# Optimization experiments

Measured on AMD Instinct MI355X. Metric: run time of the kernel, lower is better.

Reference implementation:

```python
import jax, jax.numpy as jnp
import numpy as np

B, T, S0 = 8, 4, 4096
D_MODEL, H, D, R, RANK = 2048, 16, 128, 64, 512
C = D - R  # content dim = 64


def _rope(x, positions):
    # x: [B, H, T, R]; rotate-half style RoPE as in the torch module
    half = x.shape[-1] // 2
    inv_freq = 1.0 / (10000.0 ** (jnp.arange(half, dtype=jnp.float32) / half))
    freqs = positions.astype(jnp.float32)[:, None] * inv_freq[None, :]  # [T, half]
    cos = jnp.cos(freqs)[None, None].astype(x.dtype)
    sin = jnp.sin(freqs)[None, None].astype(x.dtype)
    x1, x2 = x[..., :half], x[..., half:]
    return jnp.concatenate([x1 * cos - x2 * sin, x1 * sin + x2 * cos], axis=-1)


def setup_inputs() -> dict:
    key = jax.random.key(0)
    ks = jax.random.split(key, 9)
    s = 0.02
    return {
        "x": jax.random.normal(ks[0], (B, T, D_MODEL), jnp.float32),
        "cache_c_kv": jax.random.normal(ks[1], (B, S0, RANK), jnp.float32),
        "cache_k_rope": jax.random.normal(ks[2], (B, S0, H, R), jnp.float32),
        "w_q": jax.random.normal(ks[3], (D_MODEL, H * C), jnp.float32) * s,
        "w_q_rope": jax.random.normal(ks[4], (D_MODEL, H * R), jnp.float32) * s,
        "w_kv_down": jax.random.normal(ks[5], (D_MODEL, RANK), jnp.float32) * s,
        "w_kv_up": jax.random.normal(ks[6], (RANK, H * D), jnp.float32) * s,
        "w_k_rope": jax.random.normal(ks[7], (D_MODEL, H * R), jnp.float32) * s,
        "w_out": jax.random.normal(ks[8], (H * D, D_MODEL), jnp.float32) * s,
    }


def reference(x, cache_c_kv, cache_k_rope, w_q, w_q_rope, w_kv_down, w_kv_up, w_k_rope, w_out):
    cache_len = cache_c_kv.shape[1]
    positions = jnp.arange(cache_len, cache_len + T)

    # queries
    q_content = (x @ w_q).reshape(B, T, H, C).transpose(0, 2, 1, 3)        # [B,H,T,C]
    q_rope = (x @ w_q_rope).reshape(B, T, H, R).transpose(0, 2, 1, 3)      # [B,H,T,R]
    q_rope = _rope(q_rope, positions)
    q = jnp.concatenate([q_content, q_rope], axis=-1)                       # [B,H,T,D]

    # new compressed kv + rope keys, append to cache
    c_kv_new = x @ w_kv_down                                                # [B,T,RANK]
    k_rope_new = (x @ w_k_rope).reshape(B, T, H, R).transpose(0, 2, 1, 3)
    k_rope_new = _rope(k_rope_new, positions).transpose(0, 2, 1, 3)         # [B,T,H,R]
    c_kv = jnp.concatenate([cache_c_kv, c_kv_new], axis=1)                  # [B,S,RANK]
    k_rope = jnp.concatenate([cache_k_rope, k_rope_new], axis=1)            # [B,S,H,R]

    # decompress full cache every step (the expensive MLA pattern)
    S = c_kv.shape[1]
    kv = (c_kv @ w_kv_up).reshape(B, S, H, D)                               # [B,S,H,D]
    k_content = kv[..., :C].transpose(0, 2, 1, 3)                           # [B,H,S,C]
    v = kv.transpose(0, 2, 1, 3)                                            # [B,H,S,D]
    k = jnp.concatenate([k_content, k_rope.transpose(0, 2, 1, 3)], axis=-1) # [B,H,S,D]

    # kv_cache present => is_prefill False => no causal mask (faithful to source)
    scale = 1.0 / jnp.sqrt(jnp.asarray(D, dtype=q.dtype))
    scores = jnp.einsum('bhtd,bhsd->bhts', q, k) * scale
    attn = jax.nn.softmax(scores, axis=-1)
    out = jnp.einsum('bhts,bhsd->bhtd', attn, v)                            # [B,H,T,D]
    out = out.transpose(0, 2, 1, 3).reshape(B, T, H * D)
    return out @ w_out                                                       # [B,T,D_MODEL]
```

## Files before the change

kernel.cpp:

```cpp
#include <hip/hip_runtime.h>
#include <hip/hip_fp16.h>
#include <cmath>

#define BB 8
#define TT 4
#define HH 16
#define DDIM 128
#define RRDIM 64
#define CCDIM 64
#define RANKC 512
#define DMODEL 2048
#define S0C 4096
#define NQ 64
#define HD 2048
#define NACT 3584
#define NSC 65
#define NG 17
#define SPAD 4160
#define SCALE_ATT 0.08838834764831845f

typedef __attribute__((ext_vector_type(8))) short bf16x8;
typedef __attribute__((ext_vector_type(4))) float f32x4;
typedef unsigned short ushortT;

#define AIDX(row, kk) ((row)*132 + (((row)>>2)<<2) + (kk))

static __device__ __forceinline__ unsigned short f2bf(float x) {
  unsigned u = __float_as_uint(x);
  u += 0x7FFFu + ((u >> 16) & 1u);
  return (unsigned short)(u >> 16);
}
static __device__ __forceinline__ unsigned pk2(float a, float b) {
  return (unsigned)f2bf(a) | ((unsigned)f2bf(b) << 16);
}
static __device__ __forceinline__ bf16x8 cvt8(const float4 a, const float4 b) {
  union { uint4 u; bf16x8 h; } r;
  r.u = make_uint4(pk2(a.x, a.y), pk2(a.z, a.w), pk2(b.x, b.y), pk2(b.z, b.w));
  return r.h;
}

__global__ __launch_bounds__(256) void k_front(const float* __restrict__ A,
                                               const float* __restrict__ w0,
                                               const float* __restrict__ w1,
                                               const float* __restrict__ w2,
                                               const float* __restrict__ w3,
                                               const float* __restrict__ cckv,
                                               float* __restrict__ part,
                                               ushortT* __restrict__ ckvT,
                                               float* __restrict__ ckvn) {
  __shared__ float shf[4352];
  const int tid = threadIdx.x;
  const int bx = blockIdx.x;
  if (bx < 448) {
    const int cb = bx % 28;
    const int k0 = (bx / 28) * 128;
    const float* W; int N, lc0, off;
    if (cb < 8)       { W = w0; N = 1024; lc0 = cb * 128;        off = 0; }
    else if (cb < 16) { W = w1; N = 1024; lc0 = (cb - 8) * 128;  off = 1024; }
    else if (cb < 20) { W = w2; N = 512;  lc0 = (cb - 16) * 128; off = 2048; }
    else              { W = w3; N = 1024; lc0 = (cb - 20) * 128; off = 2560; }
    {
      const int row = tid >> 3;
      const int kseg = (tid & 7) * 16;
      const float4* s4 = reinterpret_cast<const float4*>(A + (size_t)row * DMODEL + k0 + kseg);
      float4 v0 = s4[0], v1 = s4[1], v2 = s4[2], v3 = s4[3];
      *reinterpret_cast<float4*>(&shf[AIDX(row, kseg)])      = v0;
      *reinterpret_cast<float4*>(&shf[AIDX(row, kseg + 4)])  = v1;
      *reinterpret_cast<float4*>(&shf[AIDX(row, kseg + 8)])  = v2;
      *reinterpret_cast<float4*>(&shf[AIDX(row, kseg + 12)]) = v3;
    }
    __syncthreads();
    const int cg = tid & 31;
    const int rg = tid >> 5;
    float acc[4][4];
    #pragma unroll
    for (int r = 0; r < 4; ++r)
      #pragma unroll
      for (int c = 0; c < 4; ++c) acc[r][c] = 0.f;
    #pragma unroll 4
    for (int kk = 0; kk < 128; ++kk) {
      const float4 w4 = *reinterpret_cast<const float4*>(W + (size_t)(k0 + kk) * N + lc0 + cg * 4);
      const float wv[4] = {w4.x, w4.y, w4.z, w4.w};
      #pragma unroll
      for (int r = 0; r < 4; ++r) {
        const float av = shf[AIDX(rg * 4 + r, kk)];
        #pragma unroll
        for (int c = 0; c < 4; ++c) acc[r][c] = fmaf(av, wv[c], acc[r][c]);
      }
    }
    #pragma unroll
    for (int r = 0; r < 4; ++r) {
      float4 o = make_float4(acc[r][0], acc[r][1], acc[r][2], acc[r][3]);
      *reinterpret_cast<float4*>(part + ((size_t)(bx / 28) * 32 + rg * 4 + r) * NACT + off + lc0 + cg * 4) = o;
    }
  } else if (bx < 960) {
    ushortT* tlds = reinterpret_cast<ushortT*>(shf);
    const int idx = bx - 448;
    const int b = idx >> 6, c = idx & 63;
    const float* src = cckv + ((size_t)b * S0C + c * 64) * RANKC;
    ushortT* dstT = ckvT + ((size_t)(b * NSC + c) * RANKC) * 64;
    const int s = tid >> 2, rq = tid & 3;
    const int rloc = tid >> 1, shalf = (tid & 1) * 32;
    for (int slab = 0; slab < 4; ++slab) {
      const int r0 = slab * 128;
      #pragma unroll
      for (int i = 0; i < 8; ++i) {
        const float4 v = *reinterpret_cast<const float4*>(src + (size_t)s * RANKC + r0 + rq * 32 + i * 4);
        *reinterpret_cast<uint2*>(&tlds[s * 136 + rq * 32 + i * 4]) =
            make_uint2(pk2(v.x, v.y), pk2(v.z, v.w));
      }
      __syncthreads();
      unsigned pkv[16];
      #pragma unroll
      for (int k = 0; k < 16; ++k) {
        const unsigned t0 = tlds[(shalf + 2 * k)     * 136 + rloc];
        const unsigned t1 = tlds[(shalf + 2 * k + 1) * 136 + rloc];
        pkv[k] = t0 | (t1 << 16);
      }
      uint4* d = reinterpret_cast<uint4*>(dstT + ((size_t)(r0 + rloc)) * 64 + shalf);
      d[0] = make_uint4(pkv[0], pkv[1], pkv[2], pkv[3]);
      d[1] = make_uint4(pkv[4], pkv[5], pkv[6], pkv[7]);
      d[2] = make_uint4(pkv[8], pkv[9], pkv[10], pkv[11]);
      d[3] = make_uint4(pkv[12], pkv[13], pkv[14], pkv[15]);
      __syncthreads();
    }
  } else {
    const int b = bx - 960;
    const uint4 z = make_uint4(0, 0, 0, 0);
    uint4* p = reinterpret_cast<uint4*>(ckvT + ((size_t)(b * NSC + 64) * RANKC) * 64);
    for (int i = tid; i < 4096; i += 256) p[i] = z;
    uint4* q = reinterpret_cast<uint4*>(ckvn + ((size_t)b * 64 + 4) * RANKC);
    for (int i = tid; i < 7680; i += 256) q[i] = z;
  }
}

__global__ __launch_bounds__(256) void k_mid(const float* __restrict__ part0,
                                             const float* __restrict__ cache_kr,
                                             const float* __restrict__ wup,
                                             ushortT* __restrict__ qlat,
                                             float* __restrict__ ckvn,
                                             ushortT* __restrict__ ckvT,
                                             __half* __restrict__ rs) {
  __shared__ float smid[10880];
  const int tid = threadIdx.x;
  const int bx = blockIdx.x;
  if (bx < 1152) {
    const int bh = bx / 9, sy = bx % 9;
    const int b = bh >> 4, h = bh & 15;
    float* raw_q = smid;
    float* raw_k = smid + 256;
    float* qr_l  = smid + 512;
    float* kr_l  = smid + 768;
    {
      const int t = tid >> 6, j = tid & 63;
      const size_t rowoff = (size_t)(b * TT + t) * NACT;
      float sq = 0.f, sk = 0.f;
      #pragma unroll 4
      for (int ks = 0; ks < 16; ++ks) {
        const float* pp = part0 + (size_t)ks * (32 * NACT) + rowoff;
        sq += pp[1024 + h * 64 + j];
        sk += pp[2560 + h * 64 + j];
      }
      raw_q[t * 64 + j] = sq;
      raw_k[t * 64 + j] = sk;
    }
    __syncthreads();
    {
      const int t = tid >> 6, j = tid & 63;
      const int j2 = j & 31;
      const double inv = pow(10000.0, -(double)j2 / 32.0);
      const double fr = (double)(S0C + t) * inv;
      const float cs = (float)cos(fr), sn = (float)sin(fr);
      const float qa = raw_q[t * 64 + j], qp = raw_q[t * 64 + (j ^ 32)];
      const float ka = raw_k[t * 64 + j], kp = raw_k[t * 64 + (j ^ 32)];
      float qv, kv;
      if (j < 32) { qv = qa * cs - qp * sn; kv = ka * cs - kp * sn; }
      else        { qv = qp * sn + qa * cs; kv = kp * sn + ka * cs; }
      qr_l[t * 64 + j] = qv * SCALE_ATT;
      kr_l[t * 64 + j] = kv;
    }
    __syncthreads();
    const int ql = tid & 3;
    float4 qf[4][4];
    #pragma unroll
    for (int t = 0; t < 4; ++t)
      #pragma unroll
      for (int u = 0; u < 4; ++u)
        qf[t][u] = *reinterpret_cast<const float4*>(&qr_l[t * 64 + ql * 16 + u * 4]);
    const int s0 = sy * 512;
    #pragma unroll 1
    for (int pass = 0; pass < 8; ++pass) {
      const int s = s0 + pass * 64 + (tid >> 2);
      if (s < 4100) {
        float p[4] = {0.f, 0.f, 0.f, 0.f};
        if (s < S0C) {
          const float* krow = cache_kr + (((size_t)b * S0C + s) * HH + h) * RRDIM;
          #pragma unroll
          for (int u = 0; u < 4; ++u) {
            const float4 kv = *reinterpret_cast<const float4*>(krow + ql * 16 + u * 4);
            #pragma unroll
            for (int t = 0; t < 4; ++t)
              p[t] += kv.x * qf[t][u].x + kv.y * qf[t][u].y
                    + kv.z * qf[t][u].z + kv.w * qf[t][u].w;
          }
        } else {
          const float* krow = &kr_l[(s - S0C) * 64];
          #pragma unroll
          for (int u = 0; u < 4; ++u) {
            const float4 kv = *reinterpret_cast<const float4*>(krow + ql * 16 + u * 4);
            #pragma unroll
            for (int t = 0; t < 4; ++t)
              p[t] += kv.x * qf[t][u].x + kv.y * qf[t][u].y
                    + kv.z * qf[t][u].z + kv.w * qf[t][u].w;
          }
        }
        #pragma unroll
        for (int t = 0; t < 4; ++t) {
          p[t] += __shfl_xor(p[t], 1, 4);
          p[t] += __shfl_xor(p[t], 2, 4);
        }
        rs[((size_t)bh * 4 + ql) * SPAD + s] = __float2half(p[ql]);
      }
    }
  } else if (bx < 1216) {
    const int lx = bx - 1152;
    const int h = lx & 15;
    const int r0 = (lx >> 4) * 128;
    float* wt  = smid;
    float* a_s = smid + 8448;
    {
      const int r = tid >> 1;
      const int cseg = (tid & 1) * 32;
      const float* src = wup + (size_t)(r0 + r) * HD + h * DDIM + cseg;
      #pragma unroll
      for (int u = 0; u < 8; ++u) {
        const float4 v = *reinterpret_cast<const float4*>(src + u * 4);
        wt[(cseg + u * 4 + 0) * 132 + r] = v.x;
        wt[(cseg + u * 4 + 1) * 132 + r] = v.y;
        wt[(cseg + u * 4 + 2) * 132 + r] = v.z;
        wt[(cseg + u * 4 + 3) * 132 + r] = v.w;
      }
    }
    {
      const int bt = tid >> 3;
      const int c8 = (tid & 7) * 8;
      float v[8] = {0.f,0.f,0.f,0.f,0.f,0.f,0.f,0.f};
      #pragma unroll 4
      for (int ks = 0; ks < 16; ++ks) {
        const float4* pp = reinterpret_cast<const float4*>(
            part0 + (size_t)ks * (32 * NACT) + (size_t)bt * NACT + h * CCDIM + c8);
        const float4 x0 = pp[0], x1 = pp[1];
        v[0]+=x0.x; v[1]+=x0.y; v[2]+=x0.z; v[3]+=x0.w;
        v[4]+=x1.x; v[5]+=x1.y; v[6]+=x1.z; v[7]+=x1.w;
      }
      #pragma unroll
      for (int u = 0; u < 8; ++u) a_s[bt * 68 + c8 + u] = v[u];
    }
    __syncthreads();
    const int r = tid & 127;
    const int bth = tid >> 7;
    float acc[16];
    #pragma unroll
    for (int i = 0; i < 16; ++i) acc[i] = 0.f;
    #pragma unroll 8
    for (int c = 0; c < 64; ++c) {
      const float wv = wt[c * 132 + r];
      #pragma unroll
      for (int i = 0; i < 16; ++i)
        acc[i] = fmaf(a_s[(bth * 16 + i) * 68 + c], wv, acc[i]);
    }
    #pragma unroll
    for (int i = 0; i < 16; ++i) {
      const int bt = bth * 16 + i;
      const int b = bt >> 2, t = bt & 3;
      qlat[((size_t)(b * NQ) + h * TT + t) * RANKC + r0 + r] = f2bf(acc[i]);
    }
  } else {
    const int g = (bx - 1216) * 256 + tid;
    const int r = g & 511;
    const int bt = g >> 9;
    const int b = bt >> 2, t = bt & 3;
    float s = 0.f;
    #pragma unroll 4
    for (int ks = 0; ks < 16; ++ks)
      s += part0[(size_t)ks * (32 * NACT) + (size_t)bt * NACT + 2048 + r];
    ckvn[((size_t)b * 64 + t) * RANKC + r] = s;
    ckvT[(((size_t)(b * NSC + 64) * RANKC) + r) * 64 + t] = f2bf(s);
  }
}

__global__ __launch_bounds__(256) void k_score(
    const float* __restrict__ cckv, const float* __restrict__ ckvn,
    const ushortT* __restrict__ qlat, const __half* __restrict__ rs,
    float* __restrict__ ml, ushortT* __restrict__ Pg) {
  __shared__ ushortT PL[64 * 72];
  const int tid = threadIdx.x;
  const int wv = tid >> 6;
  const int lane = tid & 63;
  const int lm = lane & 15, lg = lane >> 4;
  const int b = blockIdx.x, chunk = blockIdx.y;
  const int qbase = wv * 16;
  const int scnt = (chunk < 64) ? 64 : TT;
  const float* bsrc = (chunk < 64)
      ? cckv + ((size_t)b * S0C + (size_t)chunk * 64) * RANKC
      : ckvn + (size_t)b * 64 * RANKC;

  const ushortT* qrow = qlat + ((size_t)b * NQ + qbase + lm) * RANKC + lg * 8;
  bf16x8 qa[16];
  #pragma unroll
  for (int ks = 0; ks < 16; ++ks)
    qa[ks] = *reinterpret_cast<const bf16x8*>(qrow + ks * 32);

  f32x4 acc[4];
  #pragma unroll
  for (int st = 0; st < 4; ++st) acc[st] = (f32x4){0.f, 0.f, 0.f, 0.f};
  #pragma unroll
  for (int ks = 0; ks < 16; ++ks) {
    #pragma unroll
    for (int st = 0; st < 4; ++st) {
      const float4* bp = reinterpret_cast<const float4*>(
          bsrc + (size_t)(st * 16 + lm) * RANKC + ks * 32 + lg * 8);
      acc[st] = __builtin_amdgcn_mfma_f32_16x16x32_bf16(qa[ks], cvt8(bp[0], bp[1]), acc[st], 0, 0, 0);
    }
  }

  #pragma unroll
  for (int reg = 0; reg < 4; ++reg) {
    const int qi = qbase + lg * 4 + reg;
    const __half* rp = rs + (((size_t)(b * HH) + (qi >> 2)) * TT + (qi & 3)) * SPAD + chunk * 64;
    float vvv[4];
    float mx = -1e30f;
    #pragma unroll
    for (int st = 0; st < 4; ++st) {
      const int sl = st * 16 + lm;
      const float val = (sl < scnt)
          ? fmaf(acc[st][reg], SCALE_ATT, __half2float(rp[sl]))
          : -1e30f;
      vvv[st] = val;
      mx = fmaxf(mx, val);
    }
    #pragma unroll
    for (int off = 1; off < 16; off <<= 1) mx = fmaxf(mx, __shfl_xor(mx, off, 16));
    float sum = 0.f;
    #pragma unroll
    for (int st = 0; st < 4; ++st) {
      const float p = __expf(vvv[st] - mx);
      vvv[st] = p;
      sum += p;
    }
    #pragma unroll
    for (int off = 1; off < 16; off <<= 1) sum += __shfl_xor(sum, off, 16);
    #pragma unroll
    for (int st = 0; st < 4; ++st)
      PL[(qbase + lg * 4 + reg) * 72 + st * 16 + lm] = f2bf(vvv[st]);
    if (lm == 0) {
      const size_t mb = (((size_t)b * NSC + chunk) * NQ + qi) * 2;
      ml[mb] = mx; ml[mb + 1] = sum;
    }
  }
  __syncthreads();
  {
    const int row = tid >> 2, seg = (tid & 3) * 16;
    const uint4* sp = reinterpret_cast<const uint4*>(&PL[row * 72 + seg]);
    uint4* dp = reinterpret_cast<uint4*>(
        Pg + ((size_t)(b * NSC + chunk) * NQ + row) * 64 + seg);
    dp[0] = sp[0]; dp[1] = sp[1];
  }
}

__global__ __launch_bounds__(256) void k_pv(
    const ushortT* __restrict__ ckvT, const ushortT* __restrict__ Pg,
    const float* __restrict__ ml, float* __restrict__ olat,
    float* __restrict__ mlg) {
  const int tid = threadIdx.x;
  const int wv = tid >> 6;
  const int lane = tid & 63;
  const int lm = lane & 15, lg = lane >> 4;
  const int b = blockIdx.x, g = blockIdx.y, rg = blockIdx.z;
  const int qbase = wv * 16;
  const int nc = (g < 16) ? 4 : 1;
  const int c0 = (g < 16) ? g * 4 : 64;

  float m_cl = -1e30f, l_cl = 0.f;
  if (lg < nc) {
    const size_t mb = (((size_t)b * NSC + c0 + lg) * NQ + qbase + lm) * 2;
    m_cl = ml[mb]; l_cl = ml[mb + 1];
  }
  float mg = fmaxf(m_cl, __shfl_xor(m_cl, 16));
  mg = fmaxf(mg, __shfl_xor(mg, 32));
  const float wgt = (lg < nc) ? __expf(m_cl - mg) : 0.f;
  float la = l_cl * wgt;
  la += __shfl_xor(la, 16);
  la += __shfl_xor(la, 32);
  if (rg == 0 && lg == 0) {
    const size_t gb = (((size_t)b * NG + g) * NQ + qbase + lm) * 2;
    mlg[gb] = mg; mlg[gb + 1] = la;
  }
  float wf[4][4];
  #pragma unroll
  for (int c = 0; c < 4; ++c)
    #pragma unroll
    for (int reg = 0; reg < 4; ++reg)
      wf[c][reg] = __shfl(wgt, c * 16 + lg * 4 + reg);

  f32x4 OACC[8];
  #pragma unroll
  for (int nt = 0; nt < 8; ++nt) OACC[nt] = (f32x4){0.f, 0.f, 0.f, 0.f};

  for (int c = 0; c < nc; ++c) {
    const ushortT* pb = Pg + ((size_t)(b * NSC + c0 + c) * NQ + qbase + lm) * 64 + lg * 8;
    const bf16x8 pa0 = *reinterpret_cast<const bf16x8*>(pb);
    const bf16x8 pa1 = *reinterpret_cast<const bf16x8*>(pb + 32);
    const ushortT* vb = ckvT + (((size_t)(b * NSC + c0 + c) * RANKC) + rg * 128 + lm) * 64 + lg * 8;
    f32x4 a2[8];
    #pragma unroll
    for (int nt = 0; nt < 8; ++nt) a2[nt] = (f32x4){0.f, 0.f, 0.f, 0.f};
    #pragma unroll
    for (int nt = 0; nt < 8; ++nt) {
      const bf16x8 b0 = *reinterpret_cast<const bf16x8*>(vb + (size_t)nt * 16 * 64);
      const bf16x8 b1 = *reinterpret_cast<const bf16x8*>(vb + (size_t)nt * 16 * 64 + 32);
      a2[nt] = __builtin_amdgcn_mfma_f32_16x16x32_bf16(pa0, b0, a2[nt], 0, 0, 0);
      a2[nt] = __builtin_amdgcn_mfma_f32_16x16x32_bf16(pa1, b1, a2[nt], 0, 0, 0);
    }
    const f32x4 wv4 = {wf[c][0], wf[c][1], wf[c][2], wf[c][3]};
    #pragma unroll
    for (int nt = 0; nt < 8; ++nt) OACC[nt] += wv4 * a2[nt];
  }

  const size_t obase = ((size_t)(b * NG + g) * NQ) * RANKC;
  #pragma unroll
  for (int nt = 0; nt < 8; ++nt)
    #pragma unroll
    for (int reg = 0; reg < 4; ++reg)
      olat[obase + (size_t)(qbase + lg * 4 + reg) * RANKC + rg * 128 + nt * 16 + lm] = OACC[nt][reg];
}

__global__ __launch_bounds__(512) void k_combF(const float* __restrict__ mlg,
                                               const float* __restrict__ olat,
                                               const float* __restrict__ wup,
                                               float* __restrict__ ohead) {
  __shared__ float wrow[4][20];
  __shared__ float att_lds[4][516];
  const int h = blockIdx.x, b = blockIdx.y;
  const int tid = threadIdx.x;
  const int wave = tid >> 6;
  const int i = wave >> 1;
  const int rhalf = wave & 1;
  const int rl = tid & 63;
  const int qi = h * TT + i;
  float m1 = -1e30f, l1 = 0.f;
  if (rl < NG) {
    const size_t base = (((size_t)b * NG + rl) * NQ + qi) * 2;
    m1 = mlg[base]; l1 = mlg[base + 1];
  }
  float M = m1;
  #pragma unroll
  for (int off = 1; off < 64; off <<= 1) M = fmaxf(M, __shfl_xor(M, off));
  float L = (rl < NG) ? l1 * __expf(m1 - M) : 0.f;
  #pragma unroll
  for (int off = 1; off < 64; off <<= 1) L += __shfl_xor(L, off);
  const float invL = 1.0f / L;
  if (rl < NG) wrow[i][rl] = __expf(m1 - M) * invL;
  __syncthreads();
  const int r0 = rhalf * 256 + rl * 4;
  float o0 = 0.f, o1 = 0.f, o2 = 0.f, o3 = 0.f;
  for (int c = 0; c < NG; ++c) {
    const float w = wrow[i][c];
    const float4 v = *reinterpret_cast<const float4*>(
        olat + (((size_t)b * NG + c) * NQ + qi) * RANKC + r0);
    o0 = fmaf(v.x, w, o0); o1 = fmaf(v.y, w, o1);
    o2 = fmaf(v.z, w, o2); o3 = fmaf(v.w, w, o3);
  }
  *reinterpret_cast<float4*>(&att_lds[i][r0]) = make_float4(o0, o1, o2, o3);
  __syncthreads();
  const int col = tid & 127;
  const int t = tid >> 7;
  float acc = 0.f;
  #pragma unroll 8
  for (int r = 0; r < RANKC; ++r)
    acc = fmaf(att_lds[t][r], wup[(size_t)r * HD + h * DDIM + col], acc);
  ohead[(size_t)(b * TT + t) * HD + h * DDIM + col] = acc;
}

__global__ __launch_bounds__(256) void k_proj(const float* __restrict__ A,
                                              const float* __restrict__ W,
                                              float* __restrict__ part,
                                              int N, int NTOT, int coloff) {
  __shared__ float a_lds[4352];
  const int tid = threadIdx.x;
  const int c0 = blockIdx.x * 128;
  const int k0 = blockIdx.y * 128;
  {
    const int row = tid >> 3;
    const int kseg = (tid & 7) * 16;
    const float4* s4 = reinterpret_cast<const float4*>(A + (size_t)row * DMODEL + k0 + kseg);
    float4 v0 = s4[0], v1 = s4[1], v2 = s4[2], v3 = s4[3];
    *reinterpret_cast<float4*>(&a_lds[AIDX(row, kseg)])      = v0;
    *reinterpret_cast<float4*>(&a_lds[AIDX(row, kseg + 4)])  = v1;
    *reinterpret_cast<float4*>(&a_lds[AIDX(row, kseg + 8)])  = v2;
    *reinterpret_cast<float4*>(&a_lds[AIDX(row, kseg + 12)]) = v3;
  }
  __syncthreads();
  const int cg = tid & 31;
  const int rg = tid >> 5;
  float acc[4][4];
  #pragma unroll
  for (int r = 0; r < 4; ++r)
    #pragma unroll
    for (int c = 0; c < 4; ++c) acc[r][c] = 0.f;
  #pragma unroll 4
  for (int kk = 0; kk < 128; ++kk) {
    const float4 w4 = *reinterpret_cast<const float4*>(W + (size_t)(k0 + kk) * N + c0 + cg * 4);
    const float wv[4] = {w4.x, w4.y, w4.z, w4.w};
    #pragma unroll
    for (int r = 0; r < 4; ++r) {
      const float av = a_lds[AIDX(rg * 4 + r, kk)];
      #pragma unroll
      for (int c = 0; c < 4; ++c) acc[r][c] = fmaf(av, wv[c], acc[r][c]);
    }
  }
  #pragma unroll
  for (int r = 0; r < 4; ++r) {
    float4 o = make_float4(acc[r][0], acc[r][1], acc[r][2], acc[r][3]);
    *reinterpret_cast<float4*>(part + ((size_t)blockIdx.y * 32 + rg * 4 + r) * NTOT + coloff + c0 + cg * 4) = o;
  }
}

__global__ __launch_bounds__(256) void k_reduce(const float* __restrict__ part,
                                                float* __restrict__ out, int total, int nsplit) {
  int g = blockIdx.x * 256 + threadIdx.x;
  if (g >= total) return;
  float s = 0.f;
  #pragma unroll 4
  for (int c = 0; c < nsplit; ++c) s += part[(size_t)c * total + g];
  out[g] = s;
}

extern "C" void kernel_launch(void* const* d_in, const int* in_sizes, int n_in,
                              void* d_out, int out_size, void* d_ws, size_t ws_size,
                              hipStream_t stream) {
  const float* x     = (const float*)d_in[0];
  const float* cckv  = (const float*)d_in[1];
  const float* ckr   = (const float*)d_in[2];
  const float* w_q   = (const float*)d_in[3];
  const float* w_qr  = (const float*)d_in[4];
  const float* w_kvd = (const float*)d_in[5];
  const float* w_kvu = (const float*)d_in[6];
  const float* w_kr  = (const float*)d_in[7];
  const float* w_out = (const float*)d_in[8];
  float* out = (float*)d_out;
  float* ws = (float*)d_ws;

  size_t off = 0;
  ushortT* qlat   = (ushortT*)(ws + off); off += 65536;
  float* ckvn     = ws + off; off += 262144;
  float* mlb      = ws + off; off += (size_t)BB * NSC * NQ * 2;
  float* mlgb     = ws + off; off += (size_t)BB * NG * NQ * 2;
  float* ohead    = ws + off; off += 65536;
  __half* rsb     = (__half*)(ws + off); off += 1064960;
  ushortT* ckvT   = (ushortT*)(ws + off); off += 8519680;
  ushortT* Pgb    = (ushortT*)(ws + off); off += 1064960;
  float* regB  = ws + off;
  float* part0 = regB;
  float* olat  = regB;
  float* part3 = regB;

  k_front<<<dim3(968), 256, 0, stream>>>(x, w_q, w_qr, w_kvd, w_kr, cckv, part0, ckvT, ckvn);
  k_mid<<<dim3(1280), 256, 0, stream>>>(part0, ckr, w_kvu, qlat, ckvn, ckvT, rsb);
  k_score<<<dim3(BB, NSC), 256, 0, stream>>>(cckv, ckvn, qlat, rsb, mlb, Pgb);
  k_pv<<<dim3(BB, NG, 4), 256, 0, stream>>>(ckvT, Pgb, mlb, olat, mlgb);
  k_combF<<<dim3(16, 8), 512, 0, stream>>>(mlgb, olat, w_kvu, ohead);
  k_proj<<<dim3(16, 16), 256, 0, stream>>>(ohead, w_out, part3, 2048, 2048, 0);
  k_reduce<<<dim3(256), 256, 0, stream>>>(part3, out, 32 * HD, 16);
}
```

Baseline: 223.6 us.

## Write row-major bf16 c_kv copy in front kernel; precompute RoPE table

The front kernel, which already converts the fp32 latent cache to a transposed bf16 layout, now also writes a row-major bf16 copy. The score kernel then reads these bf16 rows directly instead of re-reading the fp32 cache and converting on the fly. This halves the bytes the score kernel streams but adds an extra write of the whole latent cache in the front kernel. RoPE cos/sin values are computed once into a small table instead of with double-precision pow/sin/cos per thread, and the new-token latents are stored only in bf16.

```diff
diff --git a/kernel.cpp b/kernel.cpp
--- a/kernel.cpp
+++ b/kernel.cpp
@@ -33,11 +33,6 @@
 static __device__ __forceinline__ unsigned pk2(float a, float b) {
   return (unsigned)f2bf(a) | ((unsigned)f2bf(b) << 16);
 }
-static __device__ __forceinline__ bf16x8 cvt8(const float4 a, const float4 b) {
-  union { uint4 u; bf16x8 h; } r;
-  r.u = make_uint4(pk2(a.x, a.y), pk2(a.z, a.w), pk2(b.x, b.y), pk2(b.z, b.w));
-  return r.h;
-}
 
 __global__ __launch_bounds__(256) void k_front(const float* __restrict__ A,
                                                const float* __restrict__ w0,
@@ -46,8 +41,9 @@
                                                const float* __restrict__ w3,
                                                const float* __restrict__ cckv,
                                                float* __restrict__ part,
+                                               ushortT* __restrict__ ckvB,
                                                ushortT* __restrict__ ckvT,
-                                               float* __restrict__ ckvn) {
+                                               float* __restrict__ rctab) {
   __shared__ float shf[4352];
   const int tid = threadIdx.x;
   const int bx = blockIdx.x;
@@ -98,16 +94,27 @@
     const int idx = bx - 448;
     const int b = idx >> 6, c = idx & 63;
     const float* src = cckv + ((size_t)b * S0C + c * 64) * RANKC;
+    ushortT* dstB = ckvB + ((size_t)(b * NSC + c) * 64) * RANKC;
     ushortT* dstT = ckvT + ((size_t)(b * NSC + c) * RANKC) * 64;
     const int s = tid >> 2, rq = tid & 3;
     const int rloc = tid >> 1, shalf = (tid & 1) * 32;
     for (int slab = 0; slab < 4; ++slab) {
       const int r0 = slab * 128;
+      unsigned pk_arr[16];
       #pragma unroll
       for (int i = 0; i < 8; ++i) {
         const float4 v = *reinterpret_cast<const float4*>(src + (size_t)s * RANKC + r0 + rq * 32 + i * 4);
+        pk_arr[2 * i]     = pk2(v.x, v.y);
+        pk_arr[2 * i + 1] = pk2(v.z, v.w);
         *reinterpret_cast<uint2*>(&tlds[s * 136 + rq * 32 + i * 4]) =
-            make_uint2(pk2(v.x, v.y), pk2(v.z, v.w));
+            make_uint2(pk_arr[2 * i], pk_arr[2 * i + 1]);
+      }
+      {
+        uint4* db = reinterpret_cast<uint4*>(dstB + (size_t)s * RANKC + r0 + rq * 32);
+        db[0] = make_uint4(pk_arr[0], pk_arr[1], pk_arr[2], pk_arr[3]);
+        db[1] = make_uint4(pk_arr[4], pk_arr[5], pk_arr[6], pk_arr[7]);
+        db[2] = make_uint4(pk_arr[8], pk_arr[9], pk_arr[10], pk_arr[11]);
+        db[3] = make_uint4(pk_arr[12], pk_arr[13], pk_arr[14], pk_arr[15]);
       }
       __syncthreads();
       unsigned pkv[16];
@@ -129,16 +136,23 @@
     const uint4 z = make_uint4(0, 0, 0, 0);
     uint4* p = reinterpret_cast<uint4*>(ckvT + ((size_t)(b * NSC + 64) * RANKC) * 64);
     for (int i = tid; i < 4096; i += 256) p[i] = z;
-    uint4* q = reinterpret_cast<uint4*>(ckvn + ((size_t)b * 64 + 4) * RANKC);
-    for (int i = tid; i < 7680; i += 256) q[i] = z;
+    uint4* q = reinterpret_cast<uint4*>(ckvB + (((size_t)(b * NSC + 64) * 64) + 4) * RANKC);
+    for (int i = tid; i < 3840; i += 256) q[i] = z;
+    if (bx == 960 && tid < 128) {
+      const int t = tid >> 5, j = tid & 31;
+      const double fr = (double)(S0C + t) * pow(10000.0, -(double)j / 32.0);
+      rctab[t * 32 + j]       = (float)cos(fr);
+      rctab[128 + t * 32 + j] = (float)sin(fr);
+    }
   }
 }
 
 __global__ __launch_bounds__(256) void k_mid(const float* __restrict__ part0,
                                              const float* __restrict__ cache_kr,
                                              const float* __restrict__ wup,
+                                             const float* __restrict__ rctab,
                                              ushortT* __restrict__ qlat,
-                                             float* __restrict__ ckvn,
+                                             ushortT* __restrict__ ckvB,
                                              ushortT* __restrict__ ckvT,
                                              __half* __restrict__ rs) {
   __shared__ float smid[10880];
@@ -168,9 +182,8 @@
     {
       const int t = tid >> 6, j = tid & 63;
       const int j2 = j & 31;
-      const double inv = pow(10000.0, -(double)j2 / 32.0);
-      const double fr = (double)(S0C + t) * inv;
-      const float cs = (float)cos(fr), sn = (float)sin(fr);
+      const float cs = rctab[t * 32 + j2];
+      const float sn = rctab[128 + t * 32 + j2];
       const float qa = raw_q[t * 64 + j], qp = raw_q[t * 64 + (j ^ 32)];
       const float ka = raw_k[t * 64 + j], kp = raw_k[t * 64 + (j ^ 32)];
       float qv, kv;
@@ -193,26 +206,16 @@
       const int s = s0 + pass * 64 + (tid >> 2);
       if (s < 4100) {
         float p[4] = {0.f, 0.f, 0.f, 0.f};
-        if (s < S0C) {
-          const float* krow = cache_kr + (((size_t)b * S0C + s) * HH + h) * RRDIM;
+        const float* krow = (s < S0C)
+            ? cache_kr + (((size_t)b * S0C + s) * HH + h) * RRDIM
+            : &kr_l[(s - S0C) * 64];
+        #pragma unroll
+        for (int u = 0; u < 4; ++u) {
+          const float4 kv = *reinterpret_cast<const float4*>(krow + ql * 16 + u * 4);
           #pragma unroll
-          for (int u = 0; u < 4; ++u) {
-            const float4 kv = *reinterpret_cast<const float4*>(krow + ql * 16 + u * 4);
-            #pragma unroll
-            for (int t = 0; t < 4; ++t)
-              p[t] += kv.x * qf[t][u].x + kv.y * qf[t][u].y
-                    + kv.z * qf[t][u].z + kv.w * qf[t][u].w;
-          }
-        } else {
-          const float* krow = &kr_l[(s - S0C) * 64];
-          #pragma unroll
-          for (int u = 0; u < 4; ++u) {
-            const float4 kv = *reinterpret_cast<const float4*>(krow + ql * 16 + u * 4);
-            #pragma unroll
-            for (int t = 0; t < 4; ++t)
-              p[t] += kv.x * qf[t][u].x + kv.y * qf[t][u].y
-                    + kv.z * qf[t][u].z + kv.w * qf[t][u].w;
-          }
+          for (int t = 0; t < 4; ++t)
+            p[t] += kv.x * qf[t][u].x + kv.y * qf[t][u].y
+                  + kv.z * qf[t][u].z + kv.w * qf[t][u].w;
         }
         #pragma unroll
         for (int t = 0; t < 4; ++t) {
@@ -284,15 +287,16 @@
     #pragma unroll 4
     for (int ks = 0; ks < 16; ++ks)
       s += part0[(size_t)ks * (32 * NACT) + (size_t)bt * NACT + 2048 + r];
-    ckvn[((size_t)b * 64 + t) * RANKC + r] = s;
-    ckvT[(((size_t)(b * NSC + 64) * RANKC) + r) * 64 + t] = f2bf(s);
+    const ushortT bv = f2bf(s);
+    ckvB[(((size_t)(b * NSC + 64) * 64) + t) * RANKC + r] = bv;
+    ckvT[(((size_t)(b * NSC + 64) * RANKC) + r) * 64 + t] = bv;
   }
 }
 
 __global__ __launch_bounds__(256) void k_score(
-    const float* __restrict__ cckv, const float* __restrict__ ckvn,
-    const ushortT* __restrict__ qlat, const __half* __restrict__ rs,
-    float* __restrict__ ml, ushortT* __restrict__ Pg) {
+    const ushortT* __restrict__ ckvB, const ushortT* __restrict__ qlat,
+    const __half* __restrict__ rs, float* __restrict__ ml,
+    ushortT* __restrict__ Pg) {
   __shared__ ushortT PL[64 * 72];
   const int tid = threadIdx.x;
   const int wv = tid >> 6;
@@ -301,9 +305,7 @@
   const int b = blockIdx.x, chunk = blockIdx.y;
   const int qbase = wv * 16;
   const int scnt = (chunk < 64) ? 64 : TT;
-  const float* bsrc = (chunk < 64)
-      ? cckv + ((size_t)b * S0C + (size_t)chunk * 64) * RANKC
-      : ckvn + (size_t)b * 64 * RANKC;
+  const ushortT* bsrc = ckvB + ((size_t)(b * NSC + chunk) * 64) * RANKC;
 
   const ushortT* qrow = qlat + ((size_t)b * NQ + qbase + lm) * RANKC + lg * 8;
   bf16x8 qa[16];
@@ -318,9 +320,9 @@
   for (int ks = 0; ks < 16; ++ks) {
     #pragma unroll
     for (int st = 0; st < 4; ++st) {
-      const float4* bp = reinterpret_cast<const float4*>(
+      const bf16x8 bf = *reinterpret_cast<const bf16x8*>(
           bsrc + (size_t)(st * 16 + lm) * RANKC + ks * 32 + lg * 8);
-      acc[st] = __builtin_amdgcn_mfma_f32_16x16x32_bf16(qa[ks], cvt8(bp[0], bp[1]), acc[st], 0, 0, 0);
+      acc[st] = __builtin_amdgcn_mfma_f32_16x16x32_bf16(qa[ks], bf, acc[st], 0, 0, 0);
     }
   }
 
@@ -552,12 +554,13 @@
   float* ws = (float*)d_ws;
 
   size_t off = 0;
-  ushortT* qlat   = (ushortT*)(ws + off); off += 65536;
-  float* ckvn     = ws + off; off += 262144;
+  ushortT* qlat   = (ushortT*)(ws + off); off += 131072;
   float* mlb      = ws + off; off += (size_t)BB * NSC * NQ * 2;
   float* mlgb     = ws + off; off += (size_t)BB * NG * NQ * 2;
   float* ohead    = ws + off; off += 65536;
+  float* rctab    = ws + off; off += 256;
   __half* rsb     = (__half*)(ws + off); off += 1064960;
+  ushortT* ckvB   = (ushortT*)(ws + off); off += 8519680;
   ushortT* ckvT   = (ushortT*)(ws + off); off += 8519680;
   ushortT* Pgb    = (ushortT*)(ws + off); off += 1064960;
   float* regB  = ws + off;
@@ -565,9 +568,9 @@
   float* olat  = regB;
   float* part3 = regB;
 
-  k_front<<<dim3(968), 256, 0, stream>>>(x, w_q, w_qr, w_kvd, w_kr, cckv, part0, ckvT, ckvn);
-  k_mid<<<dim3(1280), 256, 0, stream>>>(part0, ckr, w_kvu, qlat, ckvn, ckvT, rsb);
-  k_score<<<dim3(BB, NSC), 256, 0, stream>>>(cckv, ckvn, qlat, rsb, mlb, Pgb);
+  k_front<<<dim3(968), 256, 0, stream>>>(x, w_q, w_qr, w_kvd, w_kr, cckv, part0, ckvB, ckvT, rctab);
+  k_mid<<<dim3(1280), 256, 0, stream>>>(part0, ckr, w_kvu, rctab, qlat, ckvB, ckvT, rsb);
+  k_score<<<dim3(BB, NSC), 256, 0, stream>>>(ckvB, qlat, rsb, mlb, Pgb);
   k_pv<<<dim3(BB, NG, 4), 256, 0, stream>>>(ckvT, Pgb, mlb, olat, mlgb);
   k_combF<<<dim3(16, 8), 512, 0, stream>>>(mlgb, olat, w_kvu, ohead);
   k_proj<<<dim3(16, 16), 256, 0, stream>>>(ohead, w_out, part3, 2048, 2048, 0);
```

Result: faster. 213.2 us (-4.7%).
